# Optimization experiments

Hardware: AMD Instinct MI355X
Metric: run time of the kernel (lower is better)

Reference implementation:

```python
import jax, jax.numpy as jnp
import numpy as np

N_HEAD = 16


def setup_inputs() -> dict:
    key = jax.random.key(0)
    k1, k2, k3 = jax.random.split(key, 3)
    B, T, C = 4, 2048, 1024
    x = jax.random.normal(k1, (B, T, C), dtype=jnp.float32)
    Wqkv = jax.random.normal(k2, (C, 3 * C), dtype=jnp.float32) * 0.02
    Wproj = jax.random.normal(k3, (C, C), dtype=jnp.float32) * 0.02
    return {"x": x, "Wqkv": Wqkv, "Wproj": Wproj}


def reference(x, Wqkv, Wproj):
    B, T, C = x.shape
    nh = N_HEAD
    hd = C // nh
    qkv = x @ Wqkv                                  # (B, T, 3C)
    q, k, v = jnp.split(qkv, 3, axis=-1)
    # (B, T, C) -> (B, nh, T, hd)
    q = q.reshape(B, T, nh, hd).transpose(0, 2, 1, 3)
    k = k.reshape(B, T, nh, hd).transpose(0, 2, 1, 3)
    v = v.reshape(B, T, nh, hd).transpose(0, 2, 1, 3)
    # scaled dot-product attention with causal mask (past_kv=None => T_all == T)
    att = jnp.einsum("bhtd,bhsd->bhts", q, k) / jnp.sqrt(jnp.float32(hd))
    causal = jnp.tril(jnp.ones((T, T), dtype=bool))  # (T, T)
    att = jnp.where(causal[None, None, :, :], att, jnp.float32(-jnp.inf))
    att = jax.nn.softmax(att, axis=-1)              # (B, nh, T, T)
    y = jnp.einsum("bhts,bhsd->bhtd", att, v)       # (B, nh, T, hd)
    y = y.transpose(0, 2, 1, 3).reshape(B, T, C)
    y = y @ Wproj                                   # (B, T, C)
    # present_kv (detached in original)
    return y, jax.lax.stop_gradient(k), jax.lax.stop_gradient(v)
```

## Files before the change

### kernel.cpp

```cpp
#include <hip/hip_runtime.h>
#include <hip/hip_bf16.h>


typedef __bf16 bf16;
typedef __attribute__((ext_vector_type(8))) __bf16 bf16x8;
typedef __attribute__((ext_vector_type(4))) __bf16 bf16x4;
typedef __attribute__((ext_vector_type(4))) float f32x4;

#define AS_G __attribute__((address_space(1)))
#define AS_L __attribute__((address_space(3)))

#define QSCALE 0.1803368801111204f

__device__ __forceinline__ void gld_lds16(const bf16* g, bf16* l) {
  __builtin_amdgcn_global_load_lds((const AS_G void*)g, (AS_L void*)l, 16, 0, 0);
}

#define BAR() __builtin_amdgcn_s_barrier()
#define LGKM0() asm volatile("s_waitcnt lgkmcnt(0)" ::: "memory")
#define VMC(n) asm volatile("s_waitcnt vmcnt(" #n ")" ::: "memory")

__global__ __launch_bounds__(256) void k_prep(const float* __restrict__ x, bf16* __restrict__ xb,
                                              const float* __restrict__ Wqkv, bf16* __restrict__ wqkvT,
                                              const float* __restrict__ Wproj, bf16* __restrict__ wprojT) {
  __shared__ float tile[32][33];
  const int bid = blockIdx.x, tid = threadIdx.x;
  if (bid < 4096) {
    int i = (bid * 256 + tid) * 8;
    float4 a = *(const float4*)(x + i);
    float4 b = *(const float4*)(x + i + 4);
    bf16x8 o;
    o[0] = (bf16)a.x; o[1] = (bf16)a.y; o[2] = (bf16)a.z; o[3] = (bf16)a.w;
    o[4] = (bf16)b.x; o[5] = (bf16)b.y; o[6] = (bf16)b.z; o[7] = (bf16)b.w;
    *(bf16x8*)(xb + i) = o;
    return;
  }
  const float* in; bf16* out; int N, t;
  if (bid < 7168) { t = bid - 4096; N = 3072; in = Wqkv; out = wqkvT; }
  else            { t = bid - 7168; N = 1024; in = Wproj; out = wprojT; }
  const int nbx = N >> 5;
  const int bx = (t % nbx) * 32, by = (t / nbx) * 32;
  const int tx = tid & 31, ty = tid >> 5;
#pragma unroll
  for (int i = 0; i < 4; ++i)
    tile[ty + i * 8][tx] = in[(size_t)(by + ty + i * 8) * N + bx + tx];
  __syncthreads();
#pragma unroll
  for (int i = 0; i < 4; ++i)
    out[(size_t)(bx + ty + i * 8) * 1024 + by + tx] = (bf16)tile[tx][ty + i * 8];
}

__device__ __forceinline__ void gemm_main_256x128(const bf16* __restrict__ A,
                                                  const bf16* __restrict__ Bt,
                                                  int m0, int n0,
                                                  bf16* As, bf16* Bs,
                                                  f32x4 acc[4][4]) {
  const int tid = threadIdx.x;
  const int w = tid >> 6, lane = tid & 63, lo = lane & 15, hi = lane >> 4;
  const int wm = w >> 1, wn = w & 1;
  const int urow = tid >> 3;
  const int gsw = (tid & 7) ^ (urow & 7);
  const bf16* ga = A + (size_t)(m0 + urow) * 1024 + gsw * 8;
  const bf16* gb = Bt + (size_t)(n0 + urow) * 1024 + gsw * 8;
  const int p0 = hi ^ (lo & 7);
  const int aRow = wm * 64 + lo;
  const int bRow = wn * 64 + lo;

#define STAGE_A2(t, bufi, s0) do {                                                              \
    gld_lds16(ga + (size_t)(s0) * 65536 + (t) * 64,                                             \
              As + (bufi) * 16384 + (s0) * 4096 + w * 512);                                     \
    gld_lds16(ga + (size_t)((s0) + 1) * 65536 + (t) * 64,                                       \
              As + (bufi) * 16384 + ((s0) + 1) * 4096 + w * 512);                               \
  } while (0)
#define STAGE_B2(t, bufi) do {                                                                  \
    gld_lds16(gb + (t) * 64, Bs + (bufi) * 8192 + w * 512);                                     \
    gld_lds16(gb + 65536 + (t) * 64, Bs + (bufi) * 8192 + 4096 + w * 512);                      \
  } while (0)

  STAGE_A2(0, 0, 0); STAGE_A2(0, 0, 2); STAGE_B2(0, 0);
  STAGE_A2(1, 1, 0); STAGE_A2(1, 1, 2); STAGE_B2(1, 1);

  bf16x8 a[2][2], b[4][2];
  int buf = 0, sbuf = 2;
#pragma unroll 1
  for (int t = 0; t < 16; ++t) {
    if (t < 15) { VMC(6); } else { VMC(0); }
    BAR();
    const bf16* Ab = As + buf * 16384;
    const bf16* Bb = Bs + buf * 8192;

#pragma unroll
    for (int mi = 0; mi < 2; ++mi) {
      const bf16* r = Ab + (aRow + mi * 16) * 64;
      a[mi][0] = *(const bf16x8*)(r + p0 * 8);
      a[mi][1] = *(const bf16x8*)(r + (p0 ^ 4) * 8);
    }
#pragma unroll
    for (int ni = 0; ni < 2; ++ni) {
      const bf16* r = Bb + (bRow + ni * 16) * 64;
      b[ni][0] = *(const bf16x8*)(r + p0 * 8);
      b[ni][1] = *(const bf16x8*)(r + (p0 ^ 4) * 8);
    }
    if (t < 14) STAGE_A2(t + 2, sbuf, 0);
    BAR();
    __builtin_amdgcn_s_setprio(1);
#pragma unroll
    for (int ks = 0; ks < 2; ++ks)
#pragma unroll
      for (int mi = 0; mi < 2; ++mi)
#pragma unroll
        for (int ni = 0; ni < 2; ++ni)
          acc[mi][ni] = __builtin_amdgcn_mfma_f32_16x16x32_bf16(a[mi][ks], b[ni][ks], acc[mi][ni], 0, 0, 0);
    __builtin_amdgcn_s_setprio(0);
    BAR();

#pragma unroll
    for (int ni = 0; ni < 2; ++ni) {
      const bf16* r = Bb + (bRow + (ni + 2) * 16) * 64;
      b[ni + 2][0] = *(const bf16x8*)(r + p0 * 8);
      b[ni + 2][1] = *(const bf16x8*)(r + (p0 ^ 4) * 8);
    }
    if (t < 14) STAGE_A2(t + 2, sbuf, 2);
    BAR();
    __builtin_amdgcn_s_setprio(1);
#pragma unroll
    for (int ks = 0; ks < 2; ++ks)
#pragma unroll
      for (int mi = 0; mi < 2; ++mi)
#pragma unroll
        for (int ni = 0; ni < 2; ++ni)
          acc[mi][ni + 2] = __builtin_amdgcn_mfma_f32_16x16x32_bf16(a[mi][ks], b[ni + 2][ks], acc[mi][ni + 2], 0, 0, 0);
    __builtin_amdgcn_s_setprio(0);
    BAR();

#pragma unroll
    for (int mi = 0; mi < 2; ++mi) {
      const bf16* r = Ab + (aRow + (mi + 2) * 16) * 64;
      a[mi][0] = *(const bf16x8*)(r + p0 * 8);
      a[mi][1] = *(const bf16x8*)(r + (p0 ^ 4) * 8);
    }
    if (t < 14) STAGE_B2(t + 2, sbuf);
    BAR();
    __builtin_amdgcn_s_setprio(1);
#pragma unroll
    for (int ks = 0; ks < 2; ++ks)
#pragma unroll
      for (int mi = 0; mi < 2; ++mi)
#pragma unroll
        for (int ni = 0; ni < 2; ++ni)
          acc[mi + 2][ni + 2] = __builtin_amdgcn_mfma_f32_16x16x32_bf16(a[mi][ks], b[ni + 2][ks], acc[mi + 2][ni + 2], 0, 0, 0);
    __builtin_amdgcn_s_setprio(0);
    BAR();

    __builtin_amdgcn_s_setprio(1);
#pragma unroll
    for (int ks = 0; ks < 2; ++ks)
#pragma unroll
      for (int mi = 0; mi < 2; ++mi)
#pragma unroll
        for (int ni = 0; ni < 2; ++ni)
          acc[mi + 2][ni] = __builtin_amdgcn_mfma_f32_16x16x32_bf16(a[mi][ks], b[ni][ks], acc[mi + 2][ni], 0, 0, 0);
    __builtin_amdgcn_s_setprio(0);

    buf = (buf == 2) ? 0 : buf + 1;
    sbuf = (sbuf == 2) ? 0 : sbuf + 1;
  }
#undef STAGE_A2
#undef STAGE_B2
}

__global__ __launch_bounds__(512, 2) void k_gemm_qkv(const bf16* __restrict__ x,
                                                     const bf16* __restrict__ WqkvT,
                                                     bf16* __restrict__ qb, bf16* __restrict__ kb,
                                                     bf16* __restrict__ vtb,
                                                     float* __restrict__ outk, float* __restrict__ outv) {
  __shared__ bf16 As[49152], Bs[24576];
  int id = blockIdx.x;
  int swz = (id & 7) * 96 + (id >> 3);
  int by = swz / 24, bx = swz - by * 24;
  int m0 = by * 256, n0 = bx * 128;
  f32x4 acc[4][4] = {};
  gemm_main_256x128(x, WqkvT, m0, n0, As, Bs, acc);
  const int tid = threadIdx.x;
  const int w = tid >> 6, lane = tid & 63, lo = lane & 15, hi = lane >> 4;
  const int wm = w >> 1, wn = w & 1;
#pragma unroll
  for (int mi = 0; mi < 4; ++mi) {
    int growbase = m0 + wm * 64 + mi * 16 + hi * 4;
    int bb = growbase >> 11, t0 = growbase & 2047;
#pragma unroll
    for (int ni = 0; ni < 4; ++ni) {
      int gcol = n0 + wn * 64 + ni * 16 + lo;
      int part = gcol >> 10;
      int cc = gcol & 1023, h = cc >> 6, d = cc & 63;
      size_t idx0 = ((size_t)(bb * 16 + h) * 2048 + t0) * 64 + d;
      if (part == 0) {
#pragma unroll
        for (int r = 0; r < 4; ++r) qb[idx0 + (size_t)r * 64] = (bf16)(acc[mi][ni][r] * QSCALE);
      } else if (part == 1) {
#pragma unroll
        for (int r = 0; r < 4; ++r) {
          float val = acc[mi][ni][r];
          kb[idx0 + (size_t)r * 64] = (bf16)val;
          outk[idx0 + (size_t)r * 64] = val;
        }
      } else {
        bf16x4 pk;
#pragma unroll
        for (int r = 0; r < 4; ++r) {
          float val = acc[mi][ni][r];
          outv[idx0 + (size_t)r * 64] = val;
          pk[r] = (bf16)val;
        }
        *(bf16x4*)(vtb + ((size_t)(bb * 16 + h) * 64 + d) * 2048 + t0) = pk;
      }
    }
  }
}

__global__ __launch_bounds__(512, 2) void k_gemm_proj(const bf16* __restrict__ yb,
                                                      const bf16* __restrict__ WprojT,
                                                      float* __restrict__ out) {
  __shared__ bf16 As[49152], Bs[24576];
  int id = blockIdx.x;
  int swz = (id & 7) * 32 + (id >> 3);
  int by = swz >> 3, bx = swz & 7;
  int m0 = by * 256, n0 = bx * 128;
  f32x4 acc[4][4] = {};
  gemm_main_256x128(yb, WprojT, m0, n0, As, Bs, acc);
  const int tid = threadIdx.x;
  const int w = tid >> 6, lane = tid & 63, lo = lane & 15, hi = lane >> 4;
  const int wm = w >> 1, wn = w & 1;
#pragma unroll
  for (int mi = 0; mi < 4; ++mi)
#pragma unroll
    for (int ni = 0; ni < 4; ++ni)
#pragma unroll
      for (int r = 0; r < 4; ++r) {
        int grow = m0 + wm * 64 + mi * 16 + hi * 4 + r;
        int gcol = n0 + wn * 64 + ni * 16 + lo;
        out[(size_t)grow * 1024 + gcol] = acc[mi][ni][r];
      }
}

#define PSTR 76

__device__ __forceinline__ void p_store(f32x4 sacc[4], bool mask,
                                        int w, int lo, int hi, bf16* psrow) {
  if (mask) {
#pragma unroll
    for (int nt = 0; nt < 4; ++nt)
#pragma unroll
      for (int r = 0; r < 4; ++r)
        if (nt * 16 + hi * 4 + r > w * 16 + lo) sacc[nt][r] = -1e30f;
  }
#pragma unroll
  for (int nt = 0; nt < 4; ++nt) {
    bf16x4 pk;
#pragma unroll
    for (int r = 0; r < 4; ++r) pk[r] = (bf16)__builtin_amdgcn_exp2f(sacc[nt][r]);
    *(bf16x4*)(psrow + (w * 16 + lo) * PSTR + nt * 16 + hi * 4) = pk;
  }
}

__device__ __forceinline__ void write_y(bf16* __restrict__ y, int b, int h, int qrow,
                                        int hi, const f32x4 o[4], float inv) {
  size_t base = ((size_t)b * 2048 + qrow) * 1024 + h * 64;
#pragma unroll
  for (int mt = 0; mt < 4; ++mt) {
    bf16x4 yk;
#pragma unroll
    for (int r = 0; r < 4; ++r) yk[r] = (bf16)(o[mt][r] * inv);
    *(bf16x4*)(y + base + mt * 16 + hi * 4) = yk;
  }
}

__global__ __launch_bounds__(256, 4) void k_flash(const bf16* __restrict__ q,
                                                  const bf16* __restrict__ k,
                                                  const bf16* __restrict__ vt,
                                                  bf16* __restrict__ y) {
  __shared__ bf16 Ks[2 * 4096];
  __shared__ bf16 Vs[2 * 4096];
  __shared__ bf16 Ones[16 * 64];
  __shared__ bf16 Ps[128 * PSTR];
  const int bi = blockIdx.x;
  const int slot = bi >> 3;
  const int bh = (bi & 7) + 8 * (slot >> 4);
  const int v = slot & 15;
  const int j = ((bi >> 8) & 1) ? (15 - v) : v;
  const int jA = j, jB = 31 - j;
  const int tid = threadIdx.x, w = tid >> 6, lane = tid & 63, lo = lane & 15, hi = lane >> 4;
  const bf16* qp = q + (size_t)bh * 2048 * 64;
  const bf16* kp = k + (size_t)bh * 2048 * 64;
  const bf16* vtp = vt + (size_t)bh * 64 * 2048;

  {
    int rr = tid >> 4, c = (tid & 15) * 4;
    bf16x4 z;
    bf16 v1 = (rr == 0) ? (bf16)1.0f : (bf16)0.0f;
    z[0] = v1; z[1] = v1; z[2] = v1; z[3] = v1;
    *(bf16x4*)(Ones + rr * 64 + c) = z;
  }

#pragma unroll
  for (int p = 0; p < 2; ++p) {
    int u = tid + 256 * p;
    int row = u >> 3, g = (u & 7) ^ (row & 7);
    gld_lds16(kp + (size_t)row * 64 + g * 8, Ks + p * 2048 + w * 512);
    gld_lds16(vtp + (size_t)row * 2048 + g * 8, Vs + p * 2048 + w * 512);
  }

  bf16x8 qfA[2], qfB[2];
  {
    int qA = jA * 64 + w * 16 + lo;
    int qB = jB * 64 + w * 16 + lo;
    qfA[0] = *(const bf16x8*)(qp + (size_t)qA * 64 + hi * 8);
    qfA[1] = *(const bf16x8*)(qp + (size_t)qA * 64 + 32 + hi * 8);
    qfB[0] = *(const bf16x8*)(qp + (size_t)qB * 64 + hi * 8);
    qfB[1] = *(const bf16x8*)(qp + (size_t)qB * 64 + 32 + hi * 8);
  }
  f32x4 oA[4] = {}, oB[4] = {};
  f32x4 oLA = {}, oLB = {};

  VMC(0);
  BAR();

  for (int st = 0; st <= jB; ++st) {
    const int cb = (st & 1) * 4096;
    const int nb = cb ^ 4096;

    bf16x8 kf[4][2];
#pragma unroll
    for (int nt = 0; nt < 4; ++nt)
#pragma unroll
      for (int ks = 0; ks < 2; ++ks)
        kf[nt][ks] = *(const bf16x8*)(Ks + cb + (nt * 16 + lo) * 64 + ((ks * 4 + hi) ^ (lo & 7)) * 8);

    if (st < jB) {
      const int s1 = (st + 1) * 64;
#pragma unroll
      for (int p = 0; p < 2; ++p) {
        int u = tid + 256 * p;
        int row = u >> 3, g = (u & 7) ^ (row & 7);
        gld_lds16(kp + (size_t)(s1 + row) * 64 + g * 8, Ks + nb + p * 2048 + w * 512);
        gld_lds16(vtp + (size_t)row * 2048 + s1 + g * 8, Vs + nb + p * 2048 + w * 512);
      }
    }

    const bool actA = (st <= jA);
    f32x4 saccA[4] = {}, saccB[4] = {};
    __builtin_amdgcn_s_setprio(1);
    if (actA) {
#pragma unroll
      for (int nt = 0; nt < 4; ++nt)
#pragma unroll
        for (int ks = 0; ks < 2; ++ks)
          saccA[nt] = __builtin_amdgcn_mfma_f32_16x16x32_bf16(kf[nt][ks], qfA[ks], saccA[nt], 0, 0, 0);
    }
#pragma unroll
    for (int nt = 0; nt < 4; ++nt)
#pragma unroll
      for (int ks = 0; ks < 2; ++ks)
        saccB[nt] = __builtin_amdgcn_mfma_f32_16x16x32_bf16(kf[nt][ks], qfB[ks], saccB[nt], 0, 0, 0);
    __builtin_amdgcn_s_setprio(0);
    if (actA) p_store(saccA, st == jA, w, lo, hi, Ps);
    p_store(saccB, st == jB, w, lo, hi, Ps + 64 * PSTR);
    LGKM0();

    bf16x8 pfA[2], pfB[2];
#pragma unroll
    for (int ks = 0; ks < 2; ++ks) {
      pfB[ks] = *(const bf16x8*)(Ps + (64 + w * 16 + lo) * PSTR + ks * 32 + hi * 8);
      if (actA) pfA[ks] = *(const bf16x8*)(Ps + (w * 16 + lo) * PSTR + ks * 32 + hi * 8);
    }
    __builtin_amdgcn_s_setprio(1);
#pragma unroll
    for (int mt = 0; mt < 5; ++mt) {
#pragma unroll
      for (int ks = 0; ks < 2; ++ks) {
        int row = mt * 16 + lo;
        bf16x8 vf = (mt < 4)
            ? *(const bf16x8*)(Vs + cb + row * 64 + ((ks * 4 + hi) ^ (row & 7)) * 8)
            : *(const bf16x8*)(Ones + lo * 64 + ((ks * 4 + hi) ^ (lo & 7)) * 8);
        if (mt < 4) {
          oB[mt] = __builtin_amdgcn_mfma_f32_16x16x32_bf16(vf, pfB[ks], oB[mt], 0, 0, 0);
          if (actA) oA[mt] = __builtin_amdgcn_mfma_f32_16x16x32_bf16(vf, pfA[ks], oA[mt], 0, 0, 0);
        } else {
          oLB = __builtin_amdgcn_mfma_f32_16x16x32_bf16(vf, pfB[ks], oLB, 0, 0, 0);
          if (actA) oLA = __builtin_amdgcn_mfma_f32_16x16x32_bf16(vf, pfA[ks], oLA, 0, 0, 0);
        }
      }
    }
    __builtin_amdgcn_s_setprio(0);

    VMC(0);
    BAR();
  }

  const int b = bh >> 4, h = bh & 15;
  float lA = __shfl(oLA[0], lo, 64);
  float lB = __shfl(oLB[0], lo, 64);
  write_y(y, b, h, jA * 64 + w * 16 + lo, hi, oA, 1.0f / lA);
  write_y(y, b, h, jB * 64 + w * 16 + lo, hi, oB, 1.0f / lB);
}

extern "C" void kernel_launch(void* const* d_in, const int* in_sizes, int n_in,
                              void* d_out, int out_size, void* d_ws, size_t ws_size,
                              hipStream_t stream) {
  const float* x = (const float*)d_in[0];
  const float* Wqkv = (const float*)d_in[1];
  const float* Wproj = (const float*)d_in[2];
  float* out = (float*)d_out;

  const size_t YSZ = (size_t)8192 * 1024;
  char* ws = (char*)d_ws;
  bf16* xb = (bf16*)ws;      ws += (size_t)8192 * 1024 * 2;
  bf16* wqkvT = (bf16*)ws;   ws += (size_t)3072 * 1024 * 2;
  bf16* wprojT = (bf16*)ws;  ws += (size_t)1024 * 1024 * 2;
  bf16* qb = (bf16*)ws;      ws += (size_t)64 * 2048 * 64 * 2;
  bf16* kb = (bf16*)ws;      ws += (size_t)64 * 2048 * 64 * 2;
  bf16* vtb = (bf16*)ws;     ws += (size_t)64 * 2048 * 64 * 2;
  bf16* yb = (bf16*)ws;

  float* outy = out;
  float* outk = out + YSZ;
  float* outv = out + 2 * YSZ;

  k_prep<<<8192, 256, 0, stream>>>(x, xb, Wqkv, wqkvT, Wproj, wprojT);
  k_gemm_qkv<<<768, 512, 0, stream>>>(xb, wqkvT, qb, kb, vtb, outk, outv);
  k_flash<<<1024, 256, 0, stream>>>(qb, kb, vtb, yb);
  k_gemm_proj<<<256, 512, 0, stream>>>(yb, wprojT, outy);
}
```

Before: 302.3 us.

## Compute QKV GEMM transposed for vector stores; drop bf16 K copy, convert fp32 K in flash

After: 313.7 us. 1.04x slower.

```diff
diff --git a/kernel.cpp b/kernel.cpp
--- a/kernel.cpp
+++ b/kernel.cpp
@@ -169,50 +169,47 @@
 #undef STAGE_B2
 }
 
-__global__ __launch_bounds__(512, 2) void k_gemm_qkv(const bf16* __restrict__ x,
+__global__ __launch_bounds__(512, 2) void k_gemm_qkv(const bf16* __restrict__ xb,
                                                      const bf16* __restrict__ WqkvT,
-                                                     bf16* __restrict__ qb, bf16* __restrict__ kb,
+                                                     bf16* __restrict__ qb,
                                                      bf16* __restrict__ vtb,
                                                      float* __restrict__ outk, float* __restrict__ outv) {
   __shared__ bf16 As[49152], Bs[24576];
   int id = blockIdx.x;
   int swz = (id & 7) * 96 + (id >> 3);
-  int by = swz / 24, bx = swz - by * 24;
-  int m0 = by * 256, n0 = bx * 128;
+  int byx = swz / 12, bxw = swz - byx * 12;
+  int xrow0 = byx * 128, wcol0 = bxw * 256;
   f32x4 acc[4][4] = {};
-  gemm_main_256x128(x, WqkvT, m0, n0, As, Bs, acc);
+  gemm_main_256x128(WqkvT, xb, wcol0, xrow0, As, Bs, acc);
   const int tid = threadIdx.x;
   const int w = tid >> 6, lane = tid & 63, lo = lane & 15, hi = lane >> 4;
   const int wm = w >> 1, wn = w & 1;
 #pragma unroll
   for (int mi = 0; mi < 4; ++mi) {
-    int growbase = m0 + wm * 64 + mi * 16 + hi * 4;
-    int bb = growbase >> 11, t0 = growbase & 2047;
+    int gcb = wcol0 + wm * 64 + mi * 16 + hi * 4;
+    int part = gcb >> 10;
+    int cc = gcb & 1023, h = cc >> 6, d0 = cc & 63;
 #pragma unroll
     for (int ni = 0; ni < 4; ++ni) {
-      int gcol = n0 + wn * 64 + ni * 16 + lo;
-      int part = gcol >> 10;
-      int cc = gcol & 1023, h = cc >> 6, d = cc & 63;
-      size_t idx0 = ((size_t)(bb * 16 + h) * 2048 + t0) * 64 + d;
+      int grow = xrow0 + wn * 64 + ni * 16 + lo;
+      int bb = grow >> 11, t = grow & 2047;
+      size_t idx0 = ((size_t)(bb * 16 + h) * 2048 + t) * 64 + d0;
       if (part == 0) {
-#pragma unroll
-        for (int r = 0; r < 4; ++r) qb[idx0 + (size_t)r * 64] = (bf16)(acc[mi][ni][r] * QSCALE);
+        bf16x4 pk;
+#pragma unroll
+        for (int r = 0; r < 4; ++r) pk[r] = (bf16)(acc[mi][ni][r] * QSCALE);
+        *(bf16x4*)(qb + idx0) = pk;
       } else if (part == 1) {
-#pragma unroll
-        for (int r = 0; r < 4; ++r) {
-          float val = acc[mi][ni][r];
-          kb[idx0 + (size_t)r * 64] = (bf16)val;
-          outk[idx0 + (size_t)r * 64] = val;
-        }
+        float4 f;
+        f.x = acc[mi][ni][0]; f.y = acc[mi][ni][1]; f.z = acc[mi][ni][2]; f.w = acc[mi][ni][3];
+        *(float4*)(outk + idx0) = f;
       } else {
-        bf16x4 pk;
-#pragma unroll
-        for (int r = 0; r < 4; ++r) {
-          float val = acc[mi][ni][r];
-          outv[idx0 + (size_t)r * 64] = val;
-          pk[r] = (bf16)val;
-        }
-        *(bf16x4*)(vtb + ((size_t)(bb * 16 + h) * 64 + d) * 2048 + t0) = pk;
+        float4 f;
+        f.x = acc[mi][ni][0]; f.y = acc[mi][ni][1]; f.z = acc[mi][ni][2]; f.w = acc[mi][ni][3];
+        *(float4*)(outv + idx0) = f;
+#pragma unroll
+        for (int r = 0; r < 4; ++r)
+          vtb[((size_t)(bb * 16 + h) * 64 + d0 + r) * 2048 + t] = (bf16)acc[mi][ni][r];
       }
     }
   }
@@ -276,7 +273,7 @@
 }
 
 __global__ __launch_bounds__(256, 4) void k_flash(const bf16* __restrict__ q,
-                                                  const bf16* __restrict__ k,
+                                                  const float* __restrict__ kf32,
                                                   const bf16* __restrict__ vt,
                                                   bf16* __restrict__ y) {
   __shared__ bf16 Ks[2 * 4096];
@@ -291,8 +288,11 @@
   const int jA = j, jB = 31 - j;
   const int tid = threadIdx.x, w = tid >> 6, lane = tid & 63, lo = lane & 15, hi = lane >> 4;
   const bf16* qp = q + (size_t)bh * 2048 * 64;
-  const bf16* kp = k + (size_t)bh * 2048 * 64;
+  const float* kp = kf32 + (size_t)bh * 2048 * 64;
   const bf16* vtp = vt + (size_t)bh * 64 * 2048;
+
+  const int krow0 = tid >> 3, kc0 = tid & 7;
+  const int krow1 = (tid + 256) >> 3, kc1 = tid & 7;
 
   {
     int rr = tid >> 4, c = (tid & 15) * 4;
@@ -302,12 +302,18 @@
     *(bf16x4*)(Ones + rr * 64 + c) = z;
   }
 
-#pragma unroll
-  for (int p = 0; p < 2; ++p) {
-    int u = tid + 256 * p;
-    int row = u >> 3, g = (u & 7) ^ (row & 7);
-    gld_lds16(kp + (size_t)row * 64 + g * 8, Ks + p * 2048 + w * 512);
-    gld_lds16(vtp + (size_t)row * 2048 + g * 8, Vs + p * 2048 + w * 512);
+  float4 kr[4];
+  {
+    const float* s0p = kp + (size_t)krow0 * 64 + kc0 * 8;
+    const float* s1p = kp + (size_t)krow1 * 64 + kc1 * 8;
+    kr[0] = *(const float4*)s0p; kr[1] = *(const float4*)(s0p + 4);
+    kr[2] = *(const float4*)s1p; kr[3] = *(const float4*)(s1p + 4);
+#pragma unroll
+    for (int p = 0; p < 2; ++p) {
+      int u = tid + 256 * p;
+      int row = u >> 3, g = (u & 7) ^ (row & 7);
+      gld_lds16(vtp + (size_t)row * 2048 + g * 8, Vs + p * 2048 + w * 512);
+    }
   }
 
   bf16x8 qfA[2], qfB[2];
@@ -323,6 +329,17 @@
   f32x4 oLA = {}, oLB = {};
 
   VMC(0);
+  {
+#pragma unroll
+    for (int p = 0; p < 2; ++p) {
+      int row = p ? krow1 : krow0, c = p ? kc1 : kc0;
+      bf16x8 kk;
+#pragma unroll
+      for (int e = 0; e < 4; ++e) { kk[e] = (bf16)kr[2 * p][e]; kk[4 + e] = (bf16)kr[2 * p + 1][e]; }
+      *(bf16x8*)(Ks + row * 64 + (c ^ (row & 7)) * 8) = kk;
+    }
+  }
+  LGKM0();
   BAR();
 
   for (int st = 0; st <= jB; ++st) {
@@ -338,11 +355,14 @@
 
     if (st < jB) {
       const int s1 = (st + 1) * 64;
+      const float* s0p = kp + (size_t)(s1 + krow0) * 64 + kc0 * 8;
+      const float* s1p = kp + (size_t)(s1 + krow1) * 64 + kc1 * 8;
+      kr[0] = *(const float4*)s0p; kr[1] = *(const float4*)(s0p + 4);
+      kr[2] = *(const float4*)s1p; kr[3] = *(const float4*)(s1p + 4);
 #pragma unroll
       for (int p = 0; p < 2; ++p) {
         int u = tid + 256 * p;
         int row = u >> 3, g = (u & 7) ^ (row & 7);
-        gld_lds16(kp + (size_t)(s1 + row) * 64 + g * 8, Ks + nb + p * 2048 + w * 512);
         gld_lds16(vtp + (size_t)row * 2048 + s1 + g * 8, Vs + nb + p * 2048 + w * 512);
       }
     }
@@ -394,6 +414,17 @@
     __builtin_amdgcn_s_setprio(0);
 
     VMC(0);
+    if (st < jB) {
+#pragma unroll
+      for (int p = 0; p < 2; ++p) {
+        int row = p ? krow1 : krow0, c = p ? kc1 : kc0;
+        bf16x8 kk;
+#pragma unroll
+        for (int e = 0; e < 4; ++e) { kk[e] = (bf16)kr[2 * p][e]; kk[4 + e] = (bf16)kr[2 * p + 1][e]; }
+        *(bf16x8*)(Ks + nb + row * 64 + (c ^ (row & 7)) * 8) = kk;
+      }
+    }
+    LGKM0();
     BAR();
   }
 
@@ -418,7 +449,6 @@
   bf16* wqkvT = (bf16*)ws;   ws += (size_t)3072 * 1024 * 2;
   bf16* wprojT = (bf16*)ws;  ws += (size_t)1024 * 1024 * 2;
   bf16* qb = (bf16*)ws;      ws += (size_t)64 * 2048 * 64 * 2;
-  bf16* kb = (bf16*)ws;      ws += (size_t)64 * 2048 * 64 * 2;
   bf16* vtb = (bf16*)ws;     ws += (size_t)64 * 2048 * 64 * 2;
   bf16* yb = (bf16*)ws;
 
@@ -427,7 +457,7 @@
   float* outv = out + 2 * YSZ;
 
   k_prep<<<8192, 256, 0, stream>>>(x, xb, Wqkv, wqkvT, Wproj, wprojT);
-  k_gemm_qkv<<<768, 512, 0, stream>>>(xb, wqkvT, qb, kb, vtb, outk, outv);
-  k_flash<<<1024, 256, 0, stream>>>(qb, kb, vtb, yb);
+  k_gemm_qkv<<<768, 512, 0, stream>>>(xb, wqkvT, qb, vtb, outk, outv);
+  k_flash<<<1024, 256, 0, stream>>>(qb, outk, vtb, yb);
   k_gemm_proj<<<256, 512, 0, stream>>>(yb, wprojT, outy);
 }
```
